# Performance work log

Hardware: AMD Instinct MI355X
Metric: run time of the kernel (lower is better)

## Reference

```python
import jax, jax.numpy as jnp
import numpy as np

STRIDES = (8, 16, 32, 64, 128)
HS = (192, 96, 48, 24, 12)
NUM_CLASSES = 15
NUM_THETA = 18
B = 16
SCORE_THR = 0.05
IOU_THR = 0.3
MAX_DET = 1000


def setup_inputs() -> dict:
    key = jax.random.key(0)
    ks = jax.random.split(key, 20)
    inp = {}
    i = 0
    for name, c in (("cls", NUM_CLASSES), ("reg", 5), ("tc", NUM_THETA), ("tr", 1)):
        for l, h in enumerate(HS):
            inp[f"{name}_l{l}"] = jax.random.normal(ks[i], (B, c, h, h), dtype=jnp.float32)
            i += 1
    return inp


def _coords():
    # FCOS-style location centers per level, concatenated: [N, 2] (x, y)
    outs = []
    for h, s in zip(HS, STRIDES):
        c1d = jnp.arange(h, dtype=jnp.float32) * s + s // 2
        yy, xx = jnp.meshgrid(c1d, c1d, indexing="ij")
        outs.append(jnp.stack([xx.ravel(), yy.ravel()], axis=-1))
    return jnp.concatenate(outs, axis=0)


def _flatten(levels):
    # list of [B,C,h,w] -> [B, sum(h*w), C]  (permute to NHWC then reshape, as in torch)
    b = levels[0].shape[0]
    return jnp.concatenate(
        [jnp.transpose(t, (0, 2, 3, 1)).reshape(b, -1, t.shape[1]) for t in levels], axis=1
    )


def _pairwise_iou(boxes):
    # boxes [M,5] (x1,y1,x2,y2,theta); axis-aligned IoU on first 4 coords
    x1, y1, x2, y2 = boxes[:, 0], boxes[:, 1], boxes[:, 2], boxes[:, 3]
    area = jnp.clip(x2 - x1, 0.0) * jnp.clip(y2 - y1, 0.0)
    iw = jnp.clip(jnp.minimum(x2[:, None], x2[None, :]) - jnp.maximum(x1[:, None], x1[None, :]), 0.0)
    ih = jnp.clip(jnp.minimum(y2[:, None], y2[None, :]) - jnp.maximum(y1[:, None], y1[None, :]), 0.0)
    inter = iw * ih
    union = area[:, None] + area[None, :] - inter
    return inter / jnp.maximum(union, 1e-8)


def _nms_keep(boxes, valid, iou_thr):
    # greedy NMS over score-sorted boxes; returns bool keep mask [M]
    m = boxes.shape[0]
    iou = _pairwise_iou(boxes)
    idx = jnp.arange(m)

    def body(i, keep):
        sup = keep[i] & (iou[i] > iou_thr) & (idx > i)
        return keep & ~sup

    return jax.lax.fori_loop(0, m, body, valid)


def _forward(cls_levels, reg_levels, tc_levels, tr_levels):
    coords = _coords()  # [N,2]

    cls_preds = jax.nn.sigmoid(_flatten(cls_levels))          # [B,N,15]
    cls_scores = jnp.max(cls_preds, axis=-1)                   # [B,N]
    cls_classes = jnp.argmax(cls_preds, axis=-1) + 1           # [B,N]

    tc_preds = jax.nn.sigmoid(_flatten(tc_levels))             # [B,N,18]
    theta_c = (jnp.argmax(tc_preds, axis=-1) + 1)[..., None].astype(jnp.float32)  # [B,N,1]
    tr_lo = _flatten(tr_levels)                                # [B,N,1]
    theta = theta_c * 10.0 + tr_lo                             # [B,N,1]

    # reg: scale ltrb channels (0:4) by stride per level, keep angle channel raw
    reg_parts = []
    for t, s in zip(reg_levels, STRIDES):
        r = jnp.transpose(t, (0, 2, 3, 1)).reshape(t.shape[0], -1, 5)
        reg_parts.append(jnp.concatenate([r[..., :4] * float(s), r[..., 4:]], axis=-1))
    reg = jnp.concatenate(reg_parts, axis=1)                   # [B,N,5]

    x1y1 = coords[None, :, :] - reg[..., :2]
    x2y2 = coords[None, :, :] + reg[..., 2:4]
    boxes = jnp.concatenate([x1y1, x2y2, theta], axis=-1)      # [B,N,5]

    max_num = min(MAX_DET, cls_scores.shape[-1])
    top_scores, top_idx = jax.lax.top_k(cls_scores, max_num)   # sorted desc
    boxes_topk = jnp.take_along_axis(boxes, top_idx[..., None], axis=1)   # [B,M,5]
    classes_topk = jnp.take_along_axis(cls_classes, top_idx, axis=1)      # [B,M]

    valid = top_scores >= SCORE_THR
    keep = jax.vmap(lambda b, v: _nms_keep(b, v, IOU_THR))(boxes_topk, valid)  # [B,M] bool

    scores_post = top_scores * keep
    classes_post = classes_topk * keep
    boxes_post = boxes_topk * keep[..., None]
    return scores_post, classes_post, boxes_post


def reference(cls_l0, cls_l1, cls_l2, cls_l3, cls_l4,
              reg_l0, reg_l1, reg_l2, reg_l3, reg_l4,
              tc_l0, tc_l1, tc_l2, tc_l3, tc_l4,
              tr_l0, tr_l1, tr_l2, tr_l3, tr_l4):
    return _forward(
        [cls_l0, cls_l1, cls_l2, cls_l3, cls_l4],
        [reg_l0, reg_l1, reg_l2, reg_l3, reg_l4],
        [tc_l0, tc_l1, tc_l2, tc_l3, tc_l4],
        [tr_l0, tr_l1, tr_l2, tr_l3, tr_l4],
    )
```

## Files before the change

### kernel.cpp

```cpp
#include <hip/hip_runtime.h>
#include <stdint.h>

#define NCLS   15
#define NTH    18
#define BATCH  16
#define NANCH  49104
#define KTOP   1000
#define NWORDS 16
#define NBIN   32768
#define BSHIFT 15
#define CAND   2048

__device__ __forceinline__ float sigmoidf(float x) {
    return 1.0f / (1.0f + expf(-x));
}

__device__ __forceinline__ void levelOf(int i, int& lvl, int& h, int& s, int& pos) {
    if (i < 36864)      { lvl = 0; h = 192; s = 8;   pos = i; }
    else if (i < 46080) { lvl = 1; h = 96;  s = 16;  pos = i - 36864; }
    else if (i < 48384) { lvl = 2; h = 48;  s = 32;  pos = i - 46080; }
    else if (i < 48960) { lvl = 3; h = 24;  s = 64;  pos = i - 48384; }
    else                { lvl = 4; h = 12;  s = 128; pos = i - 48960; }
}

__device__ __forceinline__ unsigned long long shfl_u64(unsigned long long v, int src) {
    int lo = __shfl((int)(unsigned int)(v & 0xFFFFFFFFull), src);
    int hi = __shfl((int)(unsigned int)(v >> 32), src);
    return ((unsigned long long)(unsigned int)hi << 32) | (unsigned long long)(unsigned int)lo;
}

__device__ __forceinline__ void atomicOr64Shared(unsigned long long* p, unsigned long long v) {
    unsigned int* q = (unsigned int*)p;
    unsigned int lo = (unsigned int)v;
    unsigned int hi = (unsigned int)(v >> 32);
    if (lo) atomicOr(q, lo);
    if (hi) atomicOr(q + 1, hi);
}

__global__ __launch_bounds__(256) void k_zero(uint4* __restrict__ p, int n4)
{
    int i = blockIdx.x * 256 + threadIdx.x;
    if (i < n4) p[i] = make_uint4(0u, 0u, 0u, 0u);
}

__global__ __launch_bounds__(256) void k_scores(
    const float* __restrict__ c0, const float* __restrict__ c1,
    const float* __restrict__ c2, const float* __restrict__ c3,
    const float* __restrict__ c4,
    float* __restrict__ scores, unsigned int* __restrict__ hist)
{
    __shared__ unsigned int lh[NBIN / 2];
    const int b = blockIdx.y;
    for (int i = threadIdx.x; i < NBIN / 2; i += 256) lh[i] = 0u;
    __syncthreads();

    #pragma unroll
    for (int r = 0; r < 2; ++r) {
        int f4 = blockIdx.x * 512 + r * 256 + threadIdx.x;
        if (f4 < NANCH / 4) {
            int i = f4 * 4;
            int lvl, h, s, pos;
            levelOf(i, lvl, h, s, pos);
            int hh = h * h;
            const float* cp = (lvl == 0) ? c0 : (lvl == 1) ? c1 : (lvl == 2) ? c2
                              : (lvl == 3) ? c3 : c4;
            const float* base = cp + (size_t)b * NCLS * hh + pos;
            float4 mx = make_float4(-1e30f, -1e30f, -1e30f, -1e30f);
            #pragma unroll
            for (int c = 0; c < NCLS; ++c) {
                float4 v = *(const float4*)(base + (size_t)c * hh);
                mx.x = fmaxf(mx.x, v.x); mx.y = fmaxf(mx.y, v.y);
                mx.z = fmaxf(mx.z, v.z); mx.w = fmaxf(mx.w, v.w);
            }
            float4 sc = make_float4(sigmoidf(mx.x), sigmoidf(mx.y),
                                    sigmoidf(mx.z), sigmoidf(mx.w));
            *(float4*)(scores + (size_t)b * NANCH + i) = sc;
            unsigned int bin;
            bin = __float_as_uint(sc.x) >> BSHIFT;
            atomicAdd(&lh[bin >> 1], 1u << ((bin & 1) << 4));
            bin = __float_as_uint(sc.y) >> BSHIFT;
            atomicAdd(&lh[bin >> 1], 1u << ((bin & 1) << 4));
            bin = __float_as_uint(sc.z) >> BSHIFT;
            atomicAdd(&lh[bin >> 1], 1u << ((bin & 1) << 4));
            bin = __float_as_uint(sc.w) >> BSHIFT;
            atomicAdd(&lh[bin >> 1], 1u << ((bin & 1) << 4));
        }
    }
    __syncthreads();

    unsigned int* hb = hist + (size_t)b * NBIN;
    for (int wd = threadIdx.x; wd < NBIN / 2; wd += 256) {
        unsigned int v = lh[wd];
        if (v) {
            unsigned int lo = v & 0xFFFFu, hi = v >> 16;
            if (lo) atomicAdd(&hb[wd * 2], lo);
            if (hi) atomicAdd(&hb[wd * 2 + 1], hi);
        }
    }
}

__global__ __launch_bounds__(256) void k_findT(
    const unsigned int* __restrict__ hist, int* __restrict__ tbin)
{
    int b = blockIdx.x;
    int tid = threadIdx.x;
    const unsigned int* hb = hist + (size_t)b * NBIN;
    __shared__ unsigned int sc[256];
    __shared__ unsigned int fsc[128];
    __shared__ int s_c, s_t;

    unsigned int s = 0;
    const uint4* hv = (const uint4*)(hb + (size_t)tid * 128);
    #pragma unroll 8
    for (int k = 0; k < 32; ++k) {
        uint4 v = hv[k];
        s += v.x + v.y + v.z + v.w;
    }
    sc[tid] = s;
    if (tid == 0) { s_c = 0; s_t = 0; }
    __syncthreads();
    for (int d = 1; d < 256; d <<= 1) {
        unsigned int add = (tid + d < 256) ? sc[tid + d] : 0;
        __syncthreads();
        sc[tid] += add;
        __syncthreads();
    }
    if (sc[tid] >= (unsigned int)KTOP && (tid == 255 || sc[tid + 1] < (unsigned int)KTOP))
        s_c = tid;
    __syncthreads();
    int c = s_c;
    unsigned int hi = (c < 255) ? sc[c + 1] : 0;
    if (tid < 128) fsc[tid] = hb[c * 128 + tid];
    __syncthreads();
    for (int d = 1; d < 128; d <<= 1) {
        unsigned int add = (tid < 128 && tid + d < 128) ? fsc[tid + d] : 0;
        __syncthreads();
        if (tid < 128) fsc[tid] += add;
        __syncthreads();
    }
    if (tid < 128 && hi + fsc[tid] >= (unsigned int)KTOP &&
        (tid == 127 || hi + fsc[tid + 1] < (unsigned int)KTOP))
        s_t = tid;
    __syncthreads();
    if (tid == 0) tbin[b] = c * 128 + s_t;
}

__global__ __launch_bounds__(256) void k_compact(
    const float* __restrict__ scores, const int* __restrict__ tbin,
    int* __restrict__ cnt, unsigned long long* __restrict__ cand)
{
    const int b = blockIdx.y;
    const int t4 = blockIdx.x * 256 + threadIdx.x;
    __shared__ int lcnt;
    __shared__ int lbase;
    if (threadIdx.x == 0) lcnt = 0;
    __syncthreads();

    const int T = tbin[b];
    const bool in = (t4 < NANCH / 4);
    float4 v = make_float4(0.f, 0.f, 0.f, 0.f);
    if (in) v = *(const float4*)(scores + (size_t)b * NANCH + 4 * (size_t)t4);
    unsigned int bits[4] = { __float_as_uint(v.x), __float_as_uint(v.y),
                             __float_as_uint(v.z), __float_as_uint(v.w) };
    int rank[4];
    #pragma unroll
    for (int k = 0; k < 4; ++k) {
        bool pass = in && ((int)(bits[k] >> BSHIFT) >= T);
        rank[k] = pass ? atomicAdd(&lcnt, 1) : -1;
    }
    __syncthreads();
    if (threadIdx.x == 0) lbase = atomicAdd(&cnt[b * 16], lcnt);
    __syncthreads();
    const int base = lbase;
    #pragma unroll
    for (int k = 0; k < 4; ++k) {
        if (rank[k] >= 0) {
            int p = base + rank[k];
            if (p < CAND) {
                unsigned int idx = 4u * (unsigned int)t4 + (unsigned int)k;
                cand[(size_t)b * CAND + p] =
                    ((unsigned long long)bits[k] << 32) |
                    (unsigned long long)(0xFFFFFFFFu - idx);
            }
        }
    }
}

__global__ __launch_bounds__(256) void k_rankdec(
    const unsigned long long* __restrict__ cand, const int* __restrict__ cnt,
    const float* __restrict__ c0, const float* __restrict__ c1,
    const float* __restrict__ c2, const float* __restrict__ c3,
    const float* __restrict__ c4,
    const float* __restrict__ r0, const float* __restrict__ r1,
    const float* __restrict__ r2, const float* __restrict__ r3,
    const float* __restrict__ r4,
    const float* __restrict__ t0, const float* __restrict__ t1,
    const float* __restrict__ t2, const float* __restrict__ t3,
    const float* __restrict__ t4,
    const float* __restrict__ q0, const float* __restrict__ q1,
    const float* __restrict__ q2, const float* __restrict__ q3,
    const float* __restrict__ q4,
    float* __restrict__ tsc, float* __restrict__ boxes, int* __restrict__ clstop)
{
    const int b  = blockIdx.y;
    const int ci = blockIdx.x * 256 + threadIdx.x;
    __shared__ unsigned long long keys[CAND];

    int n = cnt[b * 16]; if (n > CAND) n = CAND;
    for (int i = threadIdx.x; i < CAND; i += 256)
        keys[i] = (i < n) ? cand[(size_t)b * CAND + i] : 0ull;
    __syncthreads();

    const unsigned long long my = keys[ci];
    if (my == 0ull) return;

    int rank = 0;
    #pragma unroll 8
    for (int j = 0; j < CAND; ++j)
        rank += (keys[j] > my) ? 1 : 0;
    if (rank >= KTOP) return;

    const int g   = b * KTOP + rank;
    const int idx = (int)(0xFFFFFFFFu - (unsigned int)(my & 0xFFFFFFFFull));
    tsc[g] = __uint_as_float((unsigned int)(my >> 32));

    int lvl, h, s, pos;
    levelOf(idx, lvl, h, s, pos);
    int y = pos / h, x = pos - y * h;
    int hh = h * h;
    const float* cp = (lvl == 0) ? c0 : (lvl == 1) ? c1 : (lvl == 2) ? c2 : (lvl == 3) ? c3 : c4;
    const float* rp = (lvl == 0) ? r0 : (lvl == 1) ? r1 : (lvl == 2) ? r2 : (lvl == 3) ? r3 : r4;
    const float* tp = (lvl == 0) ? t0 : (lvl == 1) ? t1 : (lvl == 2) ? t2 : (lvl == 3) ? t3 : t4;
    const float* qp = (lvl == 0) ? q0 : (lvl == 1) ? q1 : (lvl == 2) ? q2 : (lvl == 3) ? q3 : q4;
    int off = y * h + x;

    const float* cb = cp + (size_t)b * NCLS * hh + off;
    float bestc = -1e30f; int bc = 0;
    #pragma unroll
    for (int c = 0; c < NCLS; ++c) {
        float v = sigmoidf(cb[(size_t)c * hh]);
        if (v > bestc) { bestc = v; bc = c; }
    }
    clstop[g] = bc + 1;

    const float* tb = tp + (size_t)b * NTH * hh + off;
    float best = -1e30f; int bt = 0;
    #pragma unroll
    for (int c = 0; c < NTH; ++c) {
        float v = sigmoidf(tb[(size_t)c * hh]);
        if (v > best) { best = v; bt = c; }
    }
    float theta = (float)(bt + 1) * 10.0f + qp[(size_t)b * hh + off];

    const float* rb = rp + (size_t)b * 5 * hh + off;
    float fs = (float)s;
    float rr0 = rb[0] * fs;
    float rr1 = rb[(size_t)hh] * fs;
    float rr2 = rb[(size_t)2 * hh] * fs;
    float rr3 = rb[(size_t)3 * hh] * fs;
    float cx = (float)(x * s + (s >> 1));
    float cy = (float)(y * s + (s >> 1));
    float* op = boxes + (size_t)g * 5;
    op[0] = cx - rr0;
    op[1] = cy - rr1;
    op[2] = cx + rr2;
    op[3] = cy + rr3;
    op[4] = theta;
}

__global__ __launch_bounds__(256) void k_mask(
    const float* __restrict__ boxes, unsigned long long* __restrict__ mask)
{
    const int b = blockIdx.x;
    const int by = blockIdx.y;
    __shared__ float bx1[1024], by1[1024], bx2[1024], by2[1024], bar[1024];
    for (int r = threadIdx.x; r < 1024; r += 256) {
        float x1 = 0.f, y1 = 0.f, x2 = 0.f, y2 = 0.f;
        if (r < KTOP) {
            const float* p = boxes + ((size_t)(b * KTOP + r)) * 5;
            x1 = p[0]; y1 = p[1]; x2 = p[2]; y2 = p[3];
        }
        bx1[r] = x1; by1[r] = y1; bx2[r] = x2; by2[r] = y2;
        bar[r] = fmaxf(x2 - x1, 0.0f) * fmaxf(y2 - y1, 0.0f);
    }
    __syncthreads();

    const int l  = threadIdx.x & 63;
    const int wv = threadIdx.x >> 6;
    const int i  = (by << 6) + l;
    const float x1 = bx1[i], y1 = by1[i], x2 = bx2[i], y2 = by2[i], ai = bar[i];

    for (int w = by + wv; w < NWORDS; w += 4) {
        const int j0 = w << 6;
        unsigned long long m = 0ull;
        #pragma unroll 8
        for (int jj = 0; jj < 64; ++jj) {
            const int j = j0 + jj;
            float iw = fminf(x2, bx2[j]) - fmaxf(x1, bx1[j]);
            iw = fmaxf(iw, 0.0f);
            float ih = fminf(y2, by2[j]) - fmaxf(y1, by1[j]);
            ih = fmaxf(ih, 0.0f);
            float inter = iw * ih;
            float u = ai + bar[j] - inter;
            float iou = inter / fmaxf(u, 1e-8f);
            unsigned long long bit = (iou > 0.3f && j > i) ? 1ull : 0ull;
            m |= bit << jj;
        }
        mask[(((size_t)b * 1024 + i) << 4) + w] = m;
    }
}

#define LOADROW(R, W) do {                                                          \
    const ulonglong2* rp2 = (const ulonglong2*)(mask +                              \
        (((size_t)b * 1024 + ((W) << 6) + l) << 4));                                \
    _Pragma("unroll")                                                               \
    for (int p = 0; p < 8; ++p) {                                                   \
        ulonglong2 v = rp2[p]; R[2 * p] = v.x; R[2 * p + 1] = v.y;                  \
    }                                                                               \
} while (0)

#define PROC(W, R) do {                                                             \
    const unsigned long long rowword = R[W];                                        \
    unsigned long long zr = __ballot(rowword == 0ull);                              \
    unsigned long long remw = sremv[W];                                             \
    unsigned long long pend = vw[W] & ~remw;                                        \
    unsigned long long keptm = 0ull;                                                \
    while (pend) {                                                                  \
        unsigned long long nzp = pend & ~zr;                                        \
        if (!nzp) { keptm |= pend; break; }                                         \
        int jj = __builtin_ctzll(nzp);                                              \
        unsigned long long low = (1ull << jj); low = (low << 1) - 1ull;             \
        keptm |= pend & low;                                                        \
        remw |= shfl_u64(rowword, jj);                                              \
        pend &= ~low; pend &= ~remw;                                                \
    }                                                                               \
    if (l == 0) skeep[W] = keptm;                                                   \
    if ((keptm >> l) & 1ull) {                                                      \
        _Pragma("unroll")                                                           \
        for (int w2 = (W) + 1; w2 < NWORDS; ++w2)                                   \
            if (R[w2]) atomicOr64Shared(&sremv[w2], R[w2]);                         \
    }                                                                               \
} while (0)

__global__ __launch_bounds__(64) void k_nms(
    const unsigned long long* __restrict__ mask,
    const float* __restrict__ tsc, const int* __restrict__ clstop,
    const float* __restrict__ boxes, float* __restrict__ out)
{
    const int b = blockIdx.x;
    const int l = threadIdx.x;
    __shared__ unsigned long long sremv[NWORDS];
    __shared__ unsigned long long skeep[NWORDS];

    if (l < NWORDS) sremv[l] = 0ull;

    unsigned long long vw[NWORDS];
    #pragma unroll
    for (int w = 0; w < NWORDS; ++w) {
        int i = (w << 6) + l;
        bool v = (i < KTOP) && (tsc[b * KTOP + i] >= 0.05f);
        vw[w] = __ballot(v);
    }

    unsigned long long rowA[NWORDS], rowB[NWORDS];
    LOADROW(rowA, 0);
    LOADROW(rowB, 1);   PROC(0, rowA);
    LOADROW(rowA, 2);   PROC(1, rowB);
    LOADROW(rowB, 3);   PROC(2, rowA);
    LOADROW(rowA, 4);   PROC(3, rowB);
    LOADROW(rowB, 5);   PROC(4, rowA);
    LOADROW(rowA, 6);   PROC(5, rowB);
    LOADROW(rowB, 7);   PROC(6, rowA);
    LOADROW(rowA, 8);   PROC(7, rowB);
    LOADROW(rowB, 9);   PROC(8, rowA);
    LOADROW(rowA, 10);  PROC(9, rowB);
    LOADROW(rowB, 11);  PROC(10, rowA);
    LOADROW(rowA, 12);  PROC(11, rowB);
    LOADROW(rowB, 13);  PROC(12, rowA);
    LOADROW(rowA, 14);  PROC(13, rowB);
    LOADROW(rowB, 15);  PROC(14, rowA);
    PROC(15, rowB);

    #pragma unroll
    for (int w = 0; w < NWORDS; ++w) {
        int i = (w << 6) + l;
        if (i < KTOP) {
            int g = b * KTOP + i;
            float fk = (float)((skeep[w] >> l) & 1ull);
            out[g] = tsc[g] * fk;
            out[BATCH * KTOP + g] = (float)clstop[g] * fk;
            const float* bp = boxes + (size_t)g * 5;
            float* op = out + 2 * BATCH * KTOP + (size_t)g * 5;
            op[0] = bp[0] * fk;
            op[1] = bp[1] * fk;
            op[2] = bp[2] * fk;
            op[3] = bp[3] * fk;
            op[4] = bp[4] * fk;
        }
    }
}

extern "C" void kernel_launch(void* const* d_in, const int* in_sizes, int n_in,
                              void* d_out, int out_size, void* d_ws, size_t ws_size,
                              hipStream_t stream) {
    const float* c0 = (const float*)d_in[0];
    const float* c1 = (const float*)d_in[1];
    const float* c2 = (const float*)d_in[2];
    const float* c3 = (const float*)d_in[3];
    const float* c4 = (const float*)d_in[4];
    const float* r0 = (const float*)d_in[5];
    const float* r1 = (const float*)d_in[6];
    const float* r2 = (const float*)d_in[7];
    const float* r3 = (const float*)d_in[8];
    const float* r4 = (const float*)d_in[9];
    const float* t0 = (const float*)d_in[10];
    const float* t1 = (const float*)d_in[11];
    const float* t2 = (const float*)d_in[12];
    const float* t3 = (const float*)d_in[13];
    const float* t4 = (const float*)d_in[14];
    const float* q0 = (const float*)d_in[15];
    const float* q1 = (const float*)d_in[16];
    const float* q2 = (const float*)d_in[17];
    const float* q3 = (const float*)d_in[18];
    const float* q4 = (const float*)d_in[19];

    char* ws = (char*)d_ws;
    float*              scores  = (float*)(ws + 0);
    float*              tsc     = (float*)(ws + 3142656);
    int*                clstop  = (int*)(ws + 3206656);
    float*              boxes   = (float*)(ws + 3270656);
    unsigned long long* mask    = (unsigned long long*)(ws + 3590656);
    unsigned int*       hist    = (unsigned int*)(ws + 3590656);
    unsigned long long* cand    = (unsigned long long*)(ws + 5687808);
    int*                tcnt    = (int*)(ws + 5949952);
    int*                tbin    = (int*)(ws + 5950976);
    float*              out     = (float*)d_out;

    const int n4 = 2360384 / 16;
    k_zero<<<(n4 + 255) / 256, 256, 0, stream>>>((uint4*)(ws + 3590656), n4);

    k_scores<<<dim3(24, BATCH), 256, 0, stream>>>(
        c0, c1, c2, c3, c4, scores, hist);
    k_findT<<<BATCH, 256, 0, stream>>>(hist, tbin);
    k_compact<<<dim3(48, BATCH), 256, 0, stream>>>(scores, tbin, tcnt, cand);
    k_rankdec<<<dim3(8, BATCH), 256, 0, stream>>>(
        cand, tcnt,
        c0, c1, c2, c3, c4,
        r0, r1, r2, r3, r4, t0, t1, t2, t3, t4, q0, q1, q2, q3, q4,
        tsc, boxes, clstop);
    k_mask<<<dim3(BATCH, 16), 256, 0, stream>>>(boxes, mask);
    k_nms<<<BATCH, 64, 0, stream>>>(mask, tsc, clstop, boxes, out);
}
```

Before: 122.5 us.

## Precompute class and theta argmax densely; pack score histogram into 16-bit bins

The class argmax is now computed inside the score kernel and stored per anchor as a byte. A new dense kernel computes theta (argmax bin plus regression term) for every anchor. The rank/decode kernel then reads these precomputed arrays instead of gathering 34 scattered channels per selected box. The global histogram keeps the packed 16-bit bin pairs, which halves its zeroing and global atomics. In exchange, the theta logits are read for all anchors rather than only the top-k, sigmoid runs on every class logit, and an extra kernel launch is added.

Result: slower. 136.7 us (+11.6%).

```diff
diff --git a/kernel.cpp b/kernel.cpp
--- a/kernel.cpp
+++ b/kernel.cpp
@@ -47,7 +47,8 @@
     const float* __restrict__ c0, const float* __restrict__ c1,
     const float* __restrict__ c2, const float* __restrict__ c3,
     const float* __restrict__ c4,
-    float* __restrict__ scores, unsigned int* __restrict__ hist)
+    float* __restrict__ scores, unsigned char* __restrict__ classes,
+    unsigned int* __restrict__ hist)
 {
     __shared__ unsigned int lh[NBIN / 2];
     const int b = blockIdx.y;
@@ -65,38 +66,83 @@
             const float* cp = (lvl == 0) ? c0 : (lvl == 1) ? c1 : (lvl == 2) ? c2
                               : (lvl == 3) ? c3 : c4;
             const float* base = cp + (size_t)b * NCLS * hh + pos;
-            float4 mx = make_float4(-1e30f, -1e30f, -1e30f, -1e30f);
+            float4 best = make_float4(-1e30f, -1e30f, -1e30f, -1e30f);
+            int bcx = 0, bcy = 0, bcz = 0, bcw = 0;
             #pragma unroll
             for (int c = 0; c < NCLS; ++c) {
                 float4 v = *(const float4*)(base + (size_t)c * hh);
-                mx.x = fmaxf(mx.x, v.x); mx.y = fmaxf(mx.y, v.y);
-                mx.z = fmaxf(mx.z, v.z); mx.w = fmaxf(mx.w, v.w);
+                float sx = sigmoidf(v.x), sy = sigmoidf(v.y);
+                float sz = sigmoidf(v.z), sw = sigmoidf(v.w);
+                if (sx > best.x) { best.x = sx; bcx = c; }
+                if (sy > best.y) { best.y = sy; bcy = c; }
+                if (sz > best.z) { best.z = sz; bcz = c; }
+                if (sw > best.w) { best.w = sw; bcw = c; }
             }
-            float4 sc = make_float4(sigmoidf(mx.x), sigmoidf(mx.y),
-                                    sigmoidf(mx.z), sigmoidf(mx.w));
-            *(float4*)(scores + (size_t)b * NANCH + i) = sc;
+            *(float4*)(scores + (size_t)b * NANCH + i) = best;
+            uchar4 cl = make_uchar4((unsigned char)(bcx + 1), (unsigned char)(bcy + 1),
+                                    (unsigned char)(bcz + 1), (unsigned char)(bcw + 1));
+            *(uchar4*)(classes + (size_t)b * NANCH + i) = cl;
             unsigned int bin;
-            bin = __float_as_uint(sc.x) >> BSHIFT;
+            bin = __float_as_uint(best.x) >> BSHIFT;
             atomicAdd(&lh[bin >> 1], 1u << ((bin & 1) << 4));
-            bin = __float_as_uint(sc.y) >> BSHIFT;
+            bin = __float_as_uint(best.y) >> BSHIFT;
             atomicAdd(&lh[bin >> 1], 1u << ((bin & 1) << 4));
-            bin = __float_as_uint(sc.z) >> BSHIFT;
+            bin = __float_as_uint(best.z) >> BSHIFT;
             atomicAdd(&lh[bin >> 1], 1u << ((bin & 1) << 4));
-            bin = __float_as_uint(sc.w) >> BSHIFT;
+            bin = __float_as_uint(best.w) >> BSHIFT;
             atomicAdd(&lh[bin >> 1], 1u << ((bin & 1) << 4));
         }
     }
     __syncthreads();
 
-    unsigned int* hb = hist + (size_t)b * NBIN;
+    unsigned int* hb = hist + (size_t)b * (NBIN / 2);
     for (int wd = threadIdx.x; wd < NBIN / 2; wd += 256) {
         unsigned int v = lh[wd];
-        if (v) {
-            unsigned int lo = v & 0xFFFFu, hi = v >> 16;
-            if (lo) atomicAdd(&hb[wd * 2], lo);
-            if (hi) atomicAdd(&hb[wd * 2 + 1], hi);
-        }
-    }
+        if (v) atomicAdd(&hb[wd], v);
+    }
+}
+
+__global__ __launch_bounds__(256) void k_theta(
+    const float* __restrict__ t0, const float* __restrict__ t1,
+    const float* __restrict__ t2, const float* __restrict__ t3,
+    const float* __restrict__ t4,
+    const float* __restrict__ q0, const float* __restrict__ q1,
+    const float* __restrict__ q2, const float* __restrict__ q3,
+    const float* __restrict__ q4,
+    float* __restrict__ theta)
+{
+    int g4 = blockIdx.x * 256 + threadIdx.x;
+    if (g4 >= BATCH * NANCH / 4) return;
+    int g = g4 * 4;
+    int b = g / NANCH;
+    int i = g - b * NANCH;
+    int lvl, h, s, pos;
+    levelOf(i, lvl, h, s, pos);
+    int hh = h * h;
+    const float* tp = (lvl == 0) ? t0 : (lvl == 1) ? t1 : (lvl == 2) ? t2
+                      : (lvl == 3) ? t3 : t4;
+    const float* qp = (lvl == 0) ? q0 : (lvl == 1) ? q1 : (lvl == 2) ? q2
+                      : (lvl == 3) ? q3 : q4;
+    const float* base = tp + (size_t)b * NTH * hh + pos;
+    float4 best = make_float4(-1e30f, -1e30f, -1e30f, -1e30f);
+    int btx = 0, bty = 0, btz = 0, btw = 0;
+    #pragma unroll
+    for (int c = 0; c < NTH; ++c) {
+        float4 v = *(const float4*)(base + (size_t)c * hh);
+        float sx = sigmoidf(v.x), sy = sigmoidf(v.y);
+        float sz = sigmoidf(v.z), sw = sigmoidf(v.w);
+        if (sx > best.x) { best.x = sx; btx = c; }
+        if (sy > best.y) { best.y = sy; bty = c; }
+        if (sz > best.z) { best.z = sz; btz = c; }
+        if (sw > best.w) { best.w = sw; btw = c; }
+    }
+    float4 tr = *(const float4*)(qp + (size_t)b * hh + pos);
+    float4 th;
+    th.x = (float)(btx + 1) * 10.0f + tr.x;
+    th.y = (float)(bty + 1) * 10.0f + tr.y;
+    th.z = (float)(btz + 1) * 10.0f + tr.z;
+    th.w = (float)(btw + 1) * 10.0f + tr.w;
+    *(float4*)(theta + g) = th;
 }
 
 __global__ __launch_bounds__(256) void k_findT(
@@ -104,17 +150,18 @@
 {
     int b = blockIdx.x;
     int tid = threadIdx.x;
-    const unsigned int* hb = hist + (size_t)b * NBIN;
+    const unsigned int* hb = hist + (size_t)b * (NBIN / 2);
     __shared__ unsigned int sc[256];
     __shared__ unsigned int fsc[128];
     __shared__ int s_c, s_t;
 
     unsigned int s = 0;
-    const uint4* hv = (const uint4*)(hb + (size_t)tid * 128);
-    #pragma unroll 8
-    for (int k = 0; k < 32; ++k) {
+    const uint4* hv = (const uint4*)(hb + (size_t)tid * 64);
+    #pragma unroll 4
+    for (int k = 0; k < 16; ++k) {
         uint4 v = hv[k];
-        s += v.x + v.y + v.z + v.w;
+        s += (v.x & 0xFFFFu) + (v.x >> 16) + (v.y & 0xFFFFu) + (v.y >> 16)
+           + (v.z & 0xFFFFu) + (v.z >> 16) + (v.w & 0xFFFFu) + (v.w >> 16);
     }
     sc[tid] = s;
     if (tid == 0) { s_c = 0; s_t = 0; }
@@ -130,7 +177,11 @@
     __syncthreads();
     int c = s_c;
     unsigned int hi = (c < 255) ? sc[c + 1] : 0;
-    if (tid < 128) fsc[tid] = hb[c * 128 + tid];
+    if (tid < 64) {
+        unsigned int w = hb[c * 64 + tid];
+        fsc[2 * tid]     = w & 0xFFFFu;
+        fsc[2 * tid + 1] = w >> 16;
+    }
     __syncthreads();
     for (int d = 1; d < 128; d <<= 1) {
         unsigned int add = (tid < 128 && tid + d < 128) ? fsc[tid + d] : 0;
@@ -188,18 +239,10 @@
 
 __global__ __launch_bounds__(256) void k_rankdec(
     const unsigned long long* __restrict__ cand, const int* __restrict__ cnt,
-    const float* __restrict__ c0, const float* __restrict__ c1,
-    const float* __restrict__ c2, const float* __restrict__ c3,
-    const float* __restrict__ c4,
     const float* __restrict__ r0, const float* __restrict__ r1,
     const float* __restrict__ r2, const float* __restrict__ r3,
     const float* __restrict__ r4,
-    const float* __restrict__ t0, const float* __restrict__ t1,
-    const float* __restrict__ t2, const float* __restrict__ t3,
-    const float* __restrict__ t4,
-    const float* __restrict__ q0, const float* __restrict__ q1,
-    const float* __restrict__ q2, const float* __restrict__ q3,
-    const float* __restrict__ q4,
+    const float* __restrict__ theta_all, const unsigned char* __restrict__ classes_all,
     float* __restrict__ tsc, float* __restrict__ boxes, int* __restrict__ clstop)
 {
     const int b  = blockIdx.y;
@@ -223,34 +266,15 @@
     const int g   = b * KTOP + rank;
     const int idx = (int)(0xFFFFFFFFu - (unsigned int)(my & 0xFFFFFFFFull));
     tsc[g] = __uint_as_float((unsigned int)(my >> 32));
+    clstop[g] = (int)classes_all[(size_t)b * NANCH + idx];
 
     int lvl, h, s, pos;
     levelOf(idx, lvl, h, s, pos);
     int y = pos / h, x = pos - y * h;
     int hh = h * h;
-    const float* cp = (lvl == 0) ? c0 : (lvl == 1) ? c1 : (lvl == 2) ? c2 : (lvl == 3) ? c3 : c4;
-    const float* rp = (lvl == 0) ? r0 : (lvl == 1) ? r1 : (lvl == 2) ? r2 : (lvl == 3) ? r3 : r4;
-    const float* tp = (lvl == 0) ? t0 : (lvl == 1) ? t1 : (lvl == 2) ? t2 : (lvl == 3) ? t3 : t4;
-    const float* qp = (lvl == 0) ? q0 : (lvl == 1) ? q1 : (lvl == 2) ? q2 : (lvl == 3) ? q3 : q4;
+    const float* rp = (lvl == 0) ? r0 : (lvl == 1) ? r1 : (lvl == 2) ? r2
+                      : (lvl == 3) ? r3 : r4;
     int off = y * h + x;
-
-    const float* cb = cp + (size_t)b * NCLS * hh + off;
-    float bestc = -1e30f; int bc = 0;
-    #pragma unroll
-    for (int c = 0; c < NCLS; ++c) {
-        float v = sigmoidf(cb[(size_t)c * hh]);
-        if (v > bestc) { bestc = v; bc = c; }
-    }
-    clstop[g] = bc + 1;
-
-    const float* tb = tp + (size_t)b * NTH * hh + off;
-    float best = -1e30f; int bt = 0;
-    #pragma unroll
-    for (int c = 0; c < NTH; ++c) {
-        float v = sigmoidf(tb[(size_t)c * hh]);
-        if (v > best) { best = v; bt = c; }
-    }
-    float theta = (float)(bt + 1) * 10.0f + qp[(size_t)b * hh + off];
 
     const float* rb = rp + (size_t)b * 5 * hh + off;
     float fs = (float)s;
@@ -265,7 +289,7 @@
     op[1] = cy - rr1;
     op[2] = cx + rr2;
     op[3] = cy + rr3;
-    op[4] = theta;
+    op[4] = theta_all[(size_t)b * NANCH + idx];
 }
 
 __global__ __launch_bounds__(256) void k_mask(
@@ -426,28 +450,29 @@
 
     char* ws = (char*)d_ws;
     float*              scores  = (float*)(ws + 0);
-    float*              tsc     = (float*)(ws + 3142656);
-    int*                clstop  = (int*)(ws + 3206656);
-    float*              boxes   = (float*)(ws + 3270656);
-    unsigned long long* mask    = (unsigned long long*)(ws + 3590656);
-    unsigned int*       hist    = (unsigned int*)(ws + 3590656);
-    unsigned long long* cand    = (unsigned long long*)(ws + 5687808);
-    int*                tcnt    = (int*)(ws + 5949952);
-    int*                tbin    = (int*)(ws + 5950976);
+    unsigned long long* mask    = (unsigned long long*)(ws + 0);
+    float*              theta   = (float*)(ws + 3142656);
+    unsigned char*      classes = (unsigned char*)(ws + 6285312);
+    unsigned int*       hist    = (unsigned int*)(ws + 7070976);
+    int*                tcnt    = (int*)(ws + 8119552);
+    int*                tbin    = (int*)(ws + 8120576);
+    unsigned long long* cand    = (unsigned long long*)(ws + 8120640);
+    float*              tsc     = (float*)(ws + 8382784);
+    int*                clstop  = (int*)(ws + 8446784);
+    float*              boxes   = (float*)(ws + 8510784);
     float*              out     = (float*)d_out;
 
-    const int n4 = 2360384 / 16;
-    k_zero<<<(n4 + 255) / 256, 256, 0, stream>>>((uint4*)(ws + 3590656), n4);
+    const int n4 = 1049664 / 16;
+    k_zero<<<(n4 + 255) / 256, 256, 0, stream>>>((uint4*)(ws + 7070976), n4);
 
     k_scores<<<dim3(24, BATCH), 256, 0, stream>>>(
-        c0, c1, c2, c3, c4, scores, hist);
+        c0, c1, c2, c3, c4, scores, classes, hist);
+    k_theta<<<(BATCH * NANCH / 4 + 255) / 256, 256, 0, stream>>>(
+        t0, t1, t2, t3, t4, q0, q1, q2, q3, q4, theta);
     k_findT<<<BATCH, 256, 0, stream>>>(hist, tbin);
     k_compact<<<dim3(48, BATCH), 256, 0, stream>>>(scores, tbin, tcnt, cand);
     k_rankdec<<<dim3(8, BATCH), 256, 0, stream>>>(
-        cand, tcnt,
-        c0, c1, c2, c3, c4,
-        r0, r1, r2, r3, r4, t0, t1, t2, t3, t4, q0, q1, q2, q3, q4,
-        tsc, boxes, clstop);
+        cand, tcnt, r0, r1, r2, r3, r4, theta, classes, tsc, boxes, clstop);
     k_mask<<<dim3(BATCH, 16), 256, 0, stream>>>(boxes, mask);
     k_nms<<<BATCH, 64, 0, stream>>>(mask, tsc, clstop, boxes, out);
 }
```
